# Kernel optimization log

Hardware: AMD Instinct MI355X
Metric: run time of the kernel (lower is better)

The kernel has to match this reference:

```python
import jax, jax.numpy as jnp
import numpy as np

CTX = 5  # context_len

def z_vector(x, ctx):
    # x: [B, L, E] -> [B, L, ctx*E]; slot j holds embedding of token (idx + j - ctx//2), zero-padded at edges
    half = ctx // 2
    B, L, E = x.shape
    xp = jnp.pad(x, ((0, 0), (half, half), (0, 0)))
    return jnp.concatenate([xp[:, i:i + L, :] for i in range(ctx)], axis=-1)

def setup_inputs() -> dict:
    key = jax.random.key(0)
    kq, ka, kw, kb = jax.random.split(key, 4)
    B, LQ, LA, E, F = 256, 64, 256, 300, 512
    question = jax.random.normal(kq, (B, LQ, E), dtype=jnp.float32)
    answer = jax.random.normal(ka, (B, LA, E), dtype=jnp.float32)
    W = jax.random.normal(kw, (CTX * E, F), dtype=jnp.float32) * 0.02
    b = jax.random.normal(kb, (F,), dtype=jnp.float32) * 0.02
    return {"question": question, "answer": answer, "W": W, "b": b}

def reference(question, answer, W, b):
    # Conv2d(1, F, (ctx*E, 1)) over the full-height Z vector == per-position linear map
    def branch(x):
        z = z_vector(x, CTX)                       # [B, L, ctx*E]
        out = jnp.einsum('blk,kf->bfl', z, W)      # [B, F, L]
        return out + b[None, :, None]
    return branch(question), branch(answer)
```

## Files before the change

### kernel.cpp

```cpp
#include <hip/hip_runtime.h>

#define NB   256
#define E0   300
#define EP   304
#define F_   512
#define KP   1536
#define NKT  48
#define LQ_  64
#define LA_  256

typedef __attribute__((ext_vector_type(4))) float f32x4;
typedef __attribute__((ext_vector_type(8))) short short8;

#define XQ_ELEMS (NB * (LQ_ + 4) * EP)
#define XA_ELEMS (NB * (LA_ + 4) * EP)
#define WF_ELEMS (F_ * KP)
#define OUTQ_ELEMS ((size_t)NB * F_ * LQ_)
#define XROWS (NB * (LQ_ + 4) + NB * (LA_ + 4))

__device__ __forceinline__ unsigned short f2bf(float x) {
    unsigned int u = __float_as_uint(x);
    u = u + 0x7fffu + ((u >> 16) & 1u);
    return (unsigned short)(u >> 16);
}

__global__ void prep_x(const float* __restrict__ q, const float* __restrict__ a,
                       unsigned short* __restrict__ xq, unsigned short* __restrict__ xa)
{
    int idx = blockIdx.x * 256 + threadIdx.x;
    if (idx >= XROWS * 76) return;
    int row = idx / 76;
    int col = idx - row * 76;

    const float* src;
    unsigned short* dst;
    bool valid;
    if (row < NB * (LQ_ + 4)) {
        int b = row / (LQ_ + 4), lp = row - b * (LQ_ + 4);
        dst = xq + (size_t)row * EP;
        valid = (lp >= 2 && lp < 2 + LQ_);
        src = q + ((size_t)b * LQ_ + (lp - 2)) * E0;
    } else {
        int r2 = row - NB * (LQ_ + 4);
        int b = r2 / (LA_ + 4), lp = r2 - b * (LA_ + 4);
        dst = xa + (size_t)r2 * EP;
        valid = (lp >= 2 && lp < 2 + LA_);
        src = a + ((size_t)b * LA_ + (lp - 2)) * E0;
    }
    unsigned long long pk = 0ull;
    if (valid && col < 75) {
        const float4 v = reinterpret_cast<const float4*>(src)[col];
        pk = (unsigned long long)f2bf(v.x)
           | ((unsigned long long)f2bf(v.y) << 16)
           | ((unsigned long long)f2bf(v.z) << 32)
           | ((unsigned long long)f2bf(v.w) << 48);
    }
    *reinterpret_cast<unsigned long long*>(dst + (size_t)col * 4) = pk;
}

__global__ void prep_w2(const float* __restrict__ W, unsigned short* __restrict__ wfr)
{
    int idx = blockIdx.x * 256 + threadIdx.x;
    int j    = idx & 7;
    int lane = (idx >> 3) & 63;
    int chunk = idx >> 9;
    int kc = chunk % NKT;
    int tile16 = chunk / NKT;
    int f  = tile16 * 16 + (lane & 15);
    int kp = kc * 32 + (lane >> 4) * 8 + j;
    int jj = kp / EP;
    int e  = kp - jj * EP;
    float v = (kp < 5 * EP && e < E0) ? W[(size_t)(jj * E0 + e) * F_ + f] : 0.f;
    wfr[idx] = f2bf(v);
}

__global__ __launch_bounds__(256, 2) void qa_gemm(
    const unsigned short* __restrict__ xq,
    const unsigned short* __restrict__ xa,
    const unsigned short* __restrict__ wfr,
    const float* __restrict__ bias,
    float* __restrict__ out)
{
    __shared__ __align__(16) unsigned short lds[2 * 16384];

    const int bid = blockIdx.x;
    const int wg  = (bid & 7) * 160 + (bid >> 3);

    const int ftBase = (wg & 1) * 256;
    const int lt     = wg >> 1;

    const unsigned short* xp;
    float* ob;
    int Mb, lsh, Lp;
    if (lt < 128) { Mb = lt * 128;         xp = xq; lsh = 6; Lp = LQ_ + 4; ob = out; }
    else          { Mb = (lt - 128) * 128; xp = xa; lsh = 8; Lp = LA_ + 4; ob = out + OUTQ_ELEMS; }
    const int Lv = 1 << lsh;

    const int tid  = threadIdx.x;
    const int lane = tid & 63;
    const int wid  = tid >> 6;
    const int lq   = lane >> 4;
    const int lr   = lane & 15;
    const int s_c  = (lane & 3) ^ ((lane >> 3) & 3);
    const int sub  = lane >> 2;
    const int dzA  = wid * 1024;
    const int dzB  = dzA + 512;

    const int mr0 = Mb + wid * 32 + sub;
    const int mr1 = mr0 + 16;
    const unsigned short* gZ0 = xp + (size_t)((mr0 >> lsh) * Lp + (mr0 & (Lv - 1))) * EP + s_c * 8;
    const unsigned short* gZ1 = xp + (size_t)((mr1 >> lsh) * Lp + (mr1 & (Lv - 1))) * EP + s_c * 8;

    const unsigned short* wpA0 = wfr + (size_t)((ftBase >> 4) + wid * 4 + 0) * NKT * 512 + lane * 8;
    const unsigned short* wpA1 = wfr + (size_t)((ftBase >> 4) + wid * 4 + 1) * NKT * 512 + lane * 8;
    const unsigned short* wpA2 = wfr + (size_t)((ftBase >> 4) + wid * 4 + 2) * NKT * 512 + lane * 8;
    const unsigned short* wpA3 = wfr + (size_t)((ftBase >> 4) + wid * 4 + 3) * NKT * 512 + lane * 8;
    const unsigned short* wpB0 = wpA0 + 512;
    const unsigned short* wpB1 = wpA1 + 512;
    const unsigned short* wpB2 = wpA2 + 512;
    const unsigned short* wpB3 = wpA3 + 512;

    const int cs = (lq ^ ((lr >> 1) & 3)) * 16;
    int zoff[8];
#pragma unroll
    for (int n = 0; n < 8; ++n) zoff[n] = (n * 16 + lr) * 64 + cs;

#define GLLDS(p, d) __builtin_amdgcn_global_load_lds(                               \
        (const __attribute__((address_space(1))) void*)(p),                         \
        (__attribute__((address_space(3))) void*)(d), 16, 0, 0)
#define ST8(T) do { const int rb = ((T) & 1) * 16384; const size_t ko = (size_t)(T) * 128; \
    _Pragma("unroll") for (int kb = 0; kb < 4; ++kb) {                              \
        GLLDS(gZ0 + ko + kb * 32, lds + rb + kb * 4096 + dzA);                      \
        GLLDS(gZ1 + ko + kb * 32, lds + rb + kb * 4096 + dzB); } } while (0)
#define WLOAD(dst, p) do {                                                           \
    asm volatile("global_load_dwordx4 %0, %1, off" : "=v"(dst) : "v"(p) : "memory"); \
    (p) += 1024; } while (0)
#define W4A do { WLOAD(wA[0], wpA0); WLOAD(wA[1], wpA1);                             \
                 WLOAD(wA[2], wpA2); WLOAD(wA[3], wpA3); } while (0)
#define W4B do { WLOAD(wB[0], wpB0); WLOAD(wB[1], wpB1);                             \
                 WLOAD(wB[2], wpB2); WLOAD(wB[3], wpB3); } while (0)
#define ZRD8(DST, BLK) do { _Pragma("unroll") for (int n = 0; n < 8; ++n)            \
    DST[n] = *(const short8*)(bbase + (BLK) * 8192 + zoff[n]); } while (0)
#define SB __builtin_amdgcn_sched_barrier(0)
#define FENCE(VM, LG) do {                                                           \
    asm volatile("s_waitcnt vmcnt(" #VM ") lgkmcnt(" #LG ")" ::: "memory"); SB; } while (0)
#define MFMA32K(WU, ZU) do { __builtin_amdgcn_s_setprio(1);                          \
    _Pragma("unroll") for (int mf = 0; mf < 4; ++mf)                                 \
    _Pragma("unroll") for (int nt = 0; nt < 8; ++nt)                                 \
        acc[mf][nt] = __builtin_amdgcn_mfma_f32_16x16x32_bf16(                       \
            WU[mf], ZU[nt], acc[mf][nt], 0, 0, 0);                                   \
    __builtin_amdgcn_s_setprio(0); SB; } while (0)

    f32x4 acc[4][8] = {};
    short8 zA[8], zB[8], wA[4], wB[4];

    W4A; W4B;
    ST8(0);
    asm volatile("s_waitcnt vmcnt(0)\n\ts_barrier" ::: "memory");

    for (int S = 0; S < 11; ++S) {
        ST8(S + 1);
        const char* bbase = (const char*)lds + (S & 1) * 32768;
        ZRD8(zA, 0);
         ZRD8(zB, 1); FENCE(12, 8); MFMA32K(wA, zA); W4A;
         ZRD8(zA, 2); FENCE(12, 8); MFMA32K(wB, zB); W4B;
         ZRD8(zB, 3); FENCE(4,  8); MFMA32K(wA, zA); W4A;
                      FENCE(4,  0); MFMA32K(wB, zB); W4B;
        asm volatile("s_barrier" ::: "memory");
    }
    {
        const char* bbase = (const char*)lds + 32768;
        ZRD8(zA, 0);
         ZRD8(zB, 1); FENCE(4, 8); MFMA32K(wA, zA); W4A;
         ZRD8(zA, 2); FENCE(4, 8); MFMA32K(wB, zB); W4B;
         ZRD8(zB, 3); FENCE(4, 8); MFMA32K(wA, zA);
                      FENCE(0, 0); MFMA32K(wB, zB);
    }

#undef MFMA32K
#undef FENCE
#undef SB
#undef ZRD8
#undef W4A
#undef W4B
#undef WLOAD
#undef ST8
#undef GLLDS

#pragma unroll
    for (int nt = 0; nt < 8; ++nt) {
        const int m = Mb + nt * 16 + lr;
        const int b = m >> lsh;
        const int l = m & (Lv - 1);
        float* orow = ob + ((size_t)b * F_ << lsh) + l;
#pragma unroll
        for (int mf = 0; mf < 4; ++mf) {
            const int f0 = ftBase + wid * 64 + mf * 16 + lq * 4;
            const f32x4 v = acc[mf][nt];
#pragma unroll
            for (int r = 0; r < 4; ++r)
                orow[(size_t)(f0 + r) << lsh] = v[r] + __ldg(&bias[f0 + r]);
        }
    }
}

extern "C" void kernel_launch(void* const* d_in, const int* in_sizes, int n_in,
                              void* d_out, int out_size, void* d_ws, size_t ws_size,
                              hipStream_t stream)
{
    const float* q    = (const float*)d_in[0];
    const float* a    = (const float*)d_in[1];
    const float* W    = (const float*)d_in[2];
    const float* bias = (const float*)d_in[3];
    float* out = (float*)d_out;

    unsigned short* xq  = (unsigned short*)d_ws;
    unsigned short* xa  = xq + XQ_ELEMS;
    unsigned short* wfr = xa + XA_ELEMS;

    prep_x<<<(XROWS * 76 + 255) / 256, 256, 0, stream>>>(q, a, xq, xa);
    prep_w2<<<WF_ELEMS / 256, 256, 0, stream>>>(W, wfr);
    qa_gemm<<<1280, 256, 0, stream>>>(xq, xa, wfr, bias, out);
}
```

Baseline: 152.0 us.

## Shrink GEMM M-tile to 80 rows and merge prep kernels into one launch

The GEMM M-tile drops from 128 to 80 rows, so the grid grows from 1280 to 2048 workgroups, which fills the 256 CUs evenly (8 per CU). Tiles may now straddle the question/answer boundary and batch edges, so each row's source and output address is computed per row. The two prep kernels are merged into a single launch to save launch overhead. Smaller tiles cut per-block LDS and register use but lower MFMA reuse of each W fragment and add more W reloads across blocks.

```diff
diff --git a/kernel.cpp b/kernel.cpp
--- a/kernel.cpp
+++ b/kernel.cpp
@@ -17,6 +17,8 @@
 #define WF_ELEMS (F_ * KP)
 #define OUTQ_ELEMS ((size_t)NB * F_ * LQ_)
 #define XROWS (NB * (LQ_ + 4) + NB * (LA_ + 4))
+#define XPBLK 24928
+#define WPBLK 3072
 
 __device__ __forceinline__ unsigned short f2bf(float x) {
     unsigned int u = __float_as_uint(x);
@@ -24,54 +26,54 @@
     return (unsigned short)(u >> 16);
 }
 
-__global__ void prep_x(const float* __restrict__ q, const float* __restrict__ a,
-                       unsigned short* __restrict__ xq, unsigned short* __restrict__ xa)
+__global__ void prep_all(const float* __restrict__ q, const float* __restrict__ a,
+                         const float* __restrict__ W,
+                         unsigned short* __restrict__ xq, unsigned short* __restrict__ xa,
+                         unsigned short* __restrict__ wfr)
 {
-    int idx = blockIdx.x * 256 + threadIdx.x;
-    if (idx >= XROWS * 76) return;
-    int row = idx / 76;
-    int col = idx - row * 76;
-
-    const float* src;
-    unsigned short* dst;
-    bool valid;
-    if (row < NB * (LQ_ + 4)) {
-        int b = row / (LQ_ + 4), lp = row - b * (LQ_ + 4);
-        dst = xq + (size_t)row * EP;
-        valid = (lp >= 2 && lp < 2 + LQ_);
-        src = q + ((size_t)b * LQ_ + (lp - 2)) * E0;
+    const int bid = blockIdx.x;
+    if (bid < XPBLK) {
+        int idx = bid * 256 + threadIdx.x;
+        int row = idx / 76;
+        int col = idx - row * 76;
+        const float* src;
+        unsigned short* dst;
+        bool valid;
+        if (row < NB * (LQ_ + 4)) {
+            int b = row / (LQ_ + 4), lp = row - b * (LQ_ + 4);
+            dst = xq + (size_t)row * EP;
+            valid = (lp >= 2 && lp < 2 + LQ_);
+            src = q + ((size_t)b * LQ_ + (lp - 2)) * E0;
+        } else {
+            int r2 = row - NB * (LQ_ + 4);
+            int b = r2 / (LA_ + 4), lp = r2 - b * (LA_ + 4);
+            dst = xa + (size_t)r2 * EP;
+            valid = (lp >= 2 && lp < 2 + LA_);
+            src = a + ((size_t)b * LA_ + (lp - 2)) * E0;
+        }
+        unsigned long long pk = 0ull;
+        if (valid && col < 75) {
+            const float4 v = reinterpret_cast<const float4*>(src)[col];
+            pk = (unsigned long long)f2bf(v.x)
+               | ((unsigned long long)f2bf(v.y) << 16)
+               | ((unsigned long long)f2bf(v.z) << 32)
+               | ((unsigned long long)f2bf(v.w) << 48);
+        }
+        *reinterpret_cast<unsigned long long*>(dst + (size_t)col * 4) = pk;
     } else {
-        int r2 = row - NB * (LQ_ + 4);
-        int b = r2 / (LA_ + 4), lp = r2 - b * (LA_ + 4);
-        dst = xa + (size_t)r2 * EP;
-        valid = (lp >= 2 && lp < 2 + LA_);
-        src = a + ((size_t)b * LA_ + (lp - 2)) * E0;
-    }
-    unsigned long long pk = 0ull;
-    if (valid && col < 75) {
-        const float4 v = reinterpret_cast<const float4*>(src)[col];
-        pk = (unsigned long long)f2bf(v.x)
-           | ((unsigned long long)f2bf(v.y) << 16)
-           | ((unsigned long long)f2bf(v.z) << 32)
-           | ((unsigned long long)f2bf(v.w) << 48);
-    }
-    *reinterpret_cast<unsigned long long*>(dst + (size_t)col * 4) = pk;
-}
-
-__global__ void prep_w2(const float* __restrict__ W, unsigned short* __restrict__ wfr)
-{
-    int idx = blockIdx.x * 256 + threadIdx.x;
-    int j    = idx & 7;
-    int lane = (idx >> 3) & 63;
-    int chunk = idx >> 9;
-    int kc = chunk % NKT;
-    int tile16 = chunk / NKT;
-    int f  = tile16 * 16 + (lane & 15);
-    int kp = kc * 32 + (lane >> 4) * 8 + j;
-    int jj = kp / EP;
-    int e  = kp - jj * EP;
-    float v = (kp < 5 * EP && e < E0) ? W[(size_t)(jj * E0 + e) * F_ + f] : 0.f;
-    wfr[idx] = f2bf(v);
+        int idx = (bid - XPBLK) * 256 + threadIdx.x;
+        int j    = idx & 7;
+        int lane = (idx >> 3) & 63;
+        int chunk = idx >> 9;
+        int kc = chunk % NKT;
+        int tile16 = chunk / NKT;
+        int f  = tile16 * 16 + (lane & 15);
+        int kp = kc * 32 + (lane >> 4) * 8 + j;
+        int jj = kp / EP;
+        int e  = kp - jj * EP;
+        float v = (kp < 5 * EP && e < E0) ? W[(size_t)(jj * E0 + e) * F_ + f] : 0.f;
+        wfr[idx] = f2bf(v);
+    }
 }
 
 __global__ __launch_bounds__(256, 2) void qa_gemm(
@@ -81,20 +83,13 @@
     const float* __restrict__ bias,
     float* __restrict__ out)
 {
-    __shared__ __align__(16) unsigned short lds[2 * 16384];
+    __shared__ __align__(16) unsigned short lds[2 * 10240];
 
     const int bid = blockIdx.x;
-    const int wg  = (bid & 7) * 160 + (bid >> 3);
+    const int wg  = (bid & 7) * 256 + (bid >> 3);
 
     const int ftBase = (wg & 1) * 256;
-    const int lt     = wg >> 1;
-
-    const unsigned short* xp;
-    float* ob;
-    int Mb, lsh, Lp;
-    if (lt < 128) { Mb = lt * 128;         xp = xq; lsh = 6; Lp = LQ_ + 4; ob = out; }
-    else          { Mb = (lt - 128) * 128; xp = xa; lsh = 8; Lp = LA_ + 4; ob = out + OUTQ_ELEMS; }
-    const int Lv = 1 << lsh;
+    const int Mb     = (wg >> 1) * 80;
 
     const int tid  = threadIdx.x;
     const int lane = tid & 63;
@@ -103,13 +98,28 @@
     const int lr   = lane & 15;
     const int s_c  = (lane & 3) ^ ((lane >> 3) & 3);
     const int sub  = lane >> 2;
-    const int dzA  = wid * 1024;
-    const int dzB  = dzA + 512;
-
-    const int mr0 = Mb + wid * 32 + sub;
-    const int mr1 = mr0 + 16;
-    const unsigned short* gZ0 = xp + (size_t)((mr0 >> lsh) * Lp + (mr0 & (Lv - 1))) * EP + s_c * 8;
-    const unsigned short* gZ1 = xp + (size_t)((mr1 >> lsh) * Lp + (mr1 & (Lv - 1))) * EP + s_c * 8;
+
+    const unsigned short* gzu[5];
+    int dzu[5];
+#pragma unroll
+    for (int i = 0; i < 5; ++i) {
+        const int u  = wid + 4 * i;
+        const int kb = u / 5;
+        const int rg = u - kb * 5;
+        const int m  = Mb + rg * 16 + sub;
+        const unsigned short* p;
+        if (m < 16384) { int b = m >> 6, l = m & 63;            p = xq + (size_t)(b * (LQ_ + 4) + l) * EP; }
+        else { int m2 = m - 16384; int b = m2 >> 8, l = m2 & 255; p = xa + (size_t)(b * (LA_ + 4) + l) * EP; }
+        gzu[i] = p + kb * 32 + s_c * 8;
+        dzu[i] = kb * 2560 + rg * 512;
+    }
+
+#define GLLDS(p, d) __builtin_amdgcn_global_load_lds(                               \
+        (const __attribute__((address_space(1))) void*)(p),                         \
+        (__attribute__((address_space(3))) void*)(d), 16, 0, 0)
+#define ST5(T) do { const int rb = ((T) & 1) * 10240; const size_t ko = (size_t)(T) * 128; \
+    _Pragma("unroll") for (int i = 0; i < 5; ++i)                                   \
+        GLLDS(gzu[i] + ko, lds + rb + dzu[i]); } while (0)
 
     const unsigned short* wpA0 = wfr + (size_t)((ftBase >> 4) + wid * 4 + 0) * NKT * 512 + lane * 8;
     const unsigned short* wpA1 = wfr + (size_t)((ftBase >> 4) + wid * 4 + 1) * NKT * 512 + lane * 8;
@@ -120,18 +130,6 @@
     const unsigned short* wpB2 = wpA2 + 512;
     const unsigned short* wpB3 = wpA3 + 512;
 
-    const int cs = (lq ^ ((lr >> 1) & 3)) * 16;
-    int zoff[8];
-#pragma unroll
-    for (int n = 0; n < 8; ++n) zoff[n] = (n * 16 + lr) * 64 + cs;
-
-#define GLLDS(p, d) __builtin_amdgcn_global_load_lds(                               \
-        (const __attribute__((address_space(1))) void*)(p),                         \
-        (__attribute__((address_space(3))) void*)(d), 16, 0, 0)
-#define ST8(T) do { const int rb = ((T) & 1) * 16384; const size_t ko = (size_t)(T) * 128; \
-    _Pragma("unroll") for (int kb = 0; kb < 4; ++kb) {                              \
-        GLLDS(gZ0 + ko + kb * 32, lds + rb + kb * 4096 + dzA);                      \
-        GLLDS(gZ1 + ko + kb * 32, lds + rb + kb * 4096 + dzB); } } while (0)
 #define WLOAD(dst, p) do {                                                           \
     asm volatile("global_load_dwordx4 %0, %1, off" : "=v"(dst) : "v"(p) : "memory"); \
     (p) += 1024; } while (0)
@@ -139,67 +137,76 @@
                  WLOAD(wA[2], wpA2); WLOAD(wA[3], wpA3); } while (0)
 #define W4B do { WLOAD(wB[0], wpB0); WLOAD(wB[1], wpB1);                             \
                  WLOAD(wB[2], wpB2); WLOAD(wB[3], wpB3); } while (0)
-#define ZRD8(DST, BLK) do { _Pragma("unroll") for (int n = 0; n < 8; ++n)            \
-    DST[n] = *(const short8*)(bbase + (BLK) * 8192 + zoff[n]); } while (0)
+
+    const int cs = (lq ^ ((lr >> 1) & 3)) * 16;
+    int zoff[5];
+#pragma unroll
+    for (int n = 0; n < 5; ++n) zoff[n] = (n * 16 + lr) * 64 + cs;
+
+#define ZRD5(DST, BLK) do { _Pragma("unroll") for (int n = 0; n < 5; ++n)            \
+    DST[n] = *(const short8*)(bbase + (BLK) * 5120 + zoff[n]); } while (0)
 #define SB __builtin_amdgcn_sched_barrier(0)
 #define FENCE(VM, LG) do {                                                           \
     asm volatile("s_waitcnt vmcnt(" #VM ") lgkmcnt(" #LG ")" ::: "memory"); SB; } while (0)
-#define MFMA32K(WU, ZU) do { __builtin_amdgcn_s_setprio(1);                          \
+#define MFMA20(WU, ZU) do { __builtin_amdgcn_s_setprio(1);                           \
     _Pragma("unroll") for (int mf = 0; mf < 4; ++mf)                                 \
-    _Pragma("unroll") for (int nt = 0; nt < 8; ++nt)                                 \
+    _Pragma("unroll") for (int nt = 0; nt < 5; ++nt)                                 \
         acc[mf][nt] = __builtin_amdgcn_mfma_f32_16x16x32_bf16(                       \
             WU[mf], ZU[nt], acc[mf][nt], 0, 0, 0);                                   \
     __builtin_amdgcn_s_setprio(0); SB; } while (0)
 
-    f32x4 acc[4][8] = {};
-    short8 zA[8], zB[8], wA[4], wB[4];
+    f32x4 acc[4][5] = {};
+    short8 zA[5], zB[5], wA[4], wB[4];
 
     W4A; W4B;
-    ST8(0);
+    ST5(0);
     asm volatile("s_waitcnt vmcnt(0)\n\ts_barrier" ::: "memory");
 
     for (int S = 0; S < 11; ++S) {
-        ST8(S + 1);
-        const char* bbase = (const char*)lds + (S & 1) * 32768;
-        ZRD8(zA, 0);
-         ZRD8(zB, 1); FENCE(12, 8); MFMA32K(wA, zA); W4A;
-         ZRD8(zA, 2); FENCE(12, 8); MFMA32K(wB, zB); W4B;
-         ZRD8(zB, 3); FENCE(4,  8); MFMA32K(wA, zA); W4A;
-                      FENCE(4,  0); MFMA32K(wB, zB); W4B;
+        ST5(S + 1);
+        const char* bbase = (const char*)lds + (S & 1) * 20480;
+        ZRD5(zA, 0);
+         ZRD5(zB, 1); FENCE(9, 5); MFMA20(wA, zA); W4A;
+         ZRD5(zA, 2); FENCE(9, 5); MFMA20(wB, zB); W4B;
+         ZRD5(zB, 3); FENCE(4, 5); MFMA20(wA, zA); W4A;
+                      FENCE(4, 0); MFMA20(wB, zB); W4B;
         asm volatile("s_barrier" ::: "memory");
     }
     {
-        const char* bbase = (const char*)lds + 32768;
-        ZRD8(zA, 0);
-         ZRD8(zB, 1); FENCE(4, 8); MFMA32K(wA, zA); W4A;
-         ZRD8(zA, 2); FENCE(4, 8); MFMA32K(wB, zB); W4B;
-         ZRD8(zB, 3); FENCE(4, 8); MFMA32K(wA, zA);
-                      FENCE(0, 0); MFMA32K(wB, zB);
-    }
-
-#undef MFMA32K
+        const char* bbase = (const char*)lds + 20480;
+        ZRD5(zA, 0);
+         ZRD5(zB, 1); FENCE(4, 5); MFMA20(wA, zA); W4A;
+         ZRD5(zA, 2); FENCE(4, 5); MFMA20(wB, zB); W4B;
+         ZRD5(zB, 3); FENCE(4, 5); MFMA20(wA, zA);
+                      FENCE(0, 0); MFMA20(wB, zB);
+    }
+
+#undef MFMA20
 #undef FENCE
 #undef SB
-#undef ZRD8
+#undef ZRD5
 #undef W4A
 #undef W4B
 #undef WLOAD
-#undef ST8
+#undef ST5
 #undef GLLDS
 
 #pragma unroll
-    for (int nt = 0; nt < 8; ++nt) {
+    for (int nt = 0; nt < 5; ++nt) {
         const int m = Mb + nt * 16 + lr;
-        const int b = m >> lsh;
-        const int l = m & (Lv - 1);
-        float* orow = ob + ((size_t)b * F_ << lsh) + l;
+        float* orow;
+        int sh;
+        if (m < 16384) { int b = m >> 6, l = m & 63;
+            orow = out + (((size_t)b * F_) << 6) + l; sh = 6; }
+        else { int m2 = m - 16384; int b = m2 >> 8, l = m2 & 255;
+            orow = out + OUTQ_ELEMS + (((size_t)b * F_) << 8) + l; sh = 8; }
 #pragma unroll
         for (int mf = 0; mf < 4; ++mf) {
             const int f0 = ftBase + wid * 64 + mf * 16 + lq * 4;
             const f32x4 v = acc[mf][nt];
 #pragma unroll
             for (int r = 0; r < 4; ++r)
-                orow[(size_t)(f0 + r) << lsh] = v[r] + __ldg(&bias[f0 + r]);
+                orow[(size_t)(f0 + r) << sh] = v[r] + __ldg(&bias[f0 + r]);
         }
     }
 }
@@ -218,7 +225,6 @@
     unsigned short* xa  = xq + XQ_ELEMS;
     unsigned short* wfr = xa + XA_ELEMS;
 
-    prep_x<<<(XROWS * 76 + 255) / 256, 256, 0, stream>>>(q, a, xq, xa);
-    prep_w2<<<WF_ELEMS / 256, 256, 0, stream>>>(W, wfr);
-    qa_gemm<<<1280, 256, 0, stream>>>(xq, xa, wfr, bias, out);
-}
+    prep_all<<<XPBLK + WPBLK, 256, 0, stream>>>(q, a, W, xq, xa, wfr);
+    qa_gemm<<<2048, 256, 0, stream>>>(xq, xa, wfr, bias, out);
+}
```

Result: no change. 152.6 us (+0.4%).
